# Kernel optimization log

Measured on AMD Instinct MI355X. Metric: run time of the kernel, lower is better.

The kernel has to match this reference:

```python
import jax, jax.numpy as jnp
import numpy as np
import math

D_MODEL = 512
DIM_K = 512
DIM_V = 512
N_HEADS = 8
B, S = 2, 2048


def setup_inputs() -> dict:
    key = jax.random.key(0)
    ks = jax.random.split(key, 10)
    s = 1.0 / math.sqrt(D_MODEL)
    return {
        "x": jax.random.normal(ks[0], (B, S, D_MODEL), jnp.float32),
        "y": jax.random.normal(ks[1], (B, S, D_MODEL), jnp.float32),
        # torch nn.Linear weights: [out, in]
        "q_w": jax.random.normal(ks[2], (DIM_K, D_MODEL), jnp.float32) * s,
        "q_b": jax.random.normal(ks[3], (DIM_K,), jnp.float32) * s,
        "k_w": jax.random.normal(ks[4], (DIM_K, D_MODEL), jnp.float32) * s,
        "k_b": jax.random.normal(ks[5], (DIM_K,), jnp.float32) * s,
        "v_w": jax.random.normal(ks[6], (DIM_V, D_MODEL), jnp.float32) * s,
        "v_b": jax.random.normal(ks[7], (DIM_V,), jnp.float32) * s,
        "o_w": jax.random.normal(ks[8], (D_MODEL, DIM_V), jnp.float32) * s,
        "o_b": jax.random.normal(ks[9], (D_MODEL,), jnp.float32) * s,
    }


def reference(x, y, q_w, q_b, k_w, k_b, v_w, v_b, o_w, o_b):
    b, s, _ = x.shape
    hd_k = DIM_K // N_HEADS
    hd_v = DIM_V // N_HEADS
    norm_fact = 1.0 / math.sqrt(D_MODEL)  # note: original scales by 1/sqrt(d_model)
    # torch code reshapes the flat [B,S,dim] projection row-major into [H,B,S,hd]
    Q = (x @ q_w.T + q_b).reshape(N_HEADS, b, s, hd_k)
    K = (y @ k_w.T + k_b).reshape(N_HEADS, b, s, hd_k)
    V = (y @ v_w.T + v_b).reshape(N_HEADS, b, s, hd_v)
    # scores: [H, B, Sq, Sk]
    scores = jnp.einsum("hbqd,hbkd->hbqk", Q, K) * norm_fact
    # per-row mean threshold: mask (set -inf) where score <= row mean
    thre = jnp.mean(scores, axis=-1, keepdims=True)
    scores = jnp.where(scores <= thre, -jnp.inf, scores)
    attn = jax.nn.softmax(scores, axis=-1)
    out = jnp.einsum("hbqk,hbkd->hbqd", attn, V).reshape(b, s, DIM_V)
    return out @ o_w.T + o_b
```

## Files before the change

### kernel.cpp

```cpp
#include <hip/hip_runtime.h>


typedef unsigned short ushort;
typedef unsigned int uint;

typedef __bf16  bf16x8   __attribute__((ext_vector_type(8)));
typedef float   floatx4  __attribute__((ext_vector_type(4)));
typedef float   floatx16 __attribute__((ext_vector_type(16)));
typedef float   float4v  __attribute__((ext_vector_type(4)));
typedef uint    uint4v   __attribute__((ext_vector_type(4)));
typedef ushort  ushort4v __attribute__((ext_vector_type(4)));

#define MFMA16(a,b,c) __builtin_amdgcn_mfma_f32_16x16x32_bf16((a),(b),(c),0,0,0)
#define MFMA32(a,b,c) __builtin_amdgcn_mfma_f32_32x32x16_bf16((a),(b),(c),0,0,0)

__device__ __forceinline__ float b2f(ushort u){
  union { uint i; float f; } v; v.i = ((uint)u) << 16; return v.f;
}
__device__ __forceinline__ ushort f2b(float f){
  union { float f; uint i; } v; v.f = f;
  uint r = v.i + 0x7FFFu + ((v.i >> 16) & 1u);
  return (ushort)(r >> 16);
}
__device__ __forceinline__ void split2(float f, ushort& h, ushort& l){
  h = f2b(f);
  l = f2b(f - b2f(h));
}
__device__ __forceinline__ void gload16(const ushort* g, ushort* l){
  __builtin_amdgcn_global_load_lds(
      (const __attribute__((address_space(1))) unsigned int*)g,
      (__attribute__((address_space(3))) unsigned int*)l, 16, 0, 0);
}

__global__ __launch_bounds__(256) void split_all(
    const float* __restrict__ x, const float* __restrict__ y,
    const float* __restrict__ qw, const float* __restrict__ kw,
    const float* __restrict__ vw, const float* __restrict__ ow,
    ushort* __restrict__ xhi, ushort* __restrict__ xlo,
    ushort* __restrict__ yhi, ushort* __restrict__ ylo,
    ushort* __restrict__ qwh, ushort* __restrict__ qwl,
    ushort* __restrict__ kwh, ushort* __restrict__ kwl,
    ushort* __restrict__ vwh, ushort* __restrict__ owh)
{
  int idx = blockIdx.x * 256 + threadIdx.x;
  if (idx < 1048576){
    const float* sp; ushort *hp, *lp; int i;
    if (idx < 524288){ sp = x; hp = xhi; lp = xlo; i = idx; }
    else             { sp = y; hp = yhi; lp = ylo; i = idx - 524288; }
    float4v d = ((const float4v*)sp)[i];
    ushort4v h, l;
    #pragma unroll
    for (int j=0;j<4;j++){ ushort hh,ll; split2(d[j],hh,ll); h[j]=hh; l[j]=ll; }
    ((ushort4v*)hp)[i] = h;
    ((ushort4v*)lp)[i] = l;
  } else {
    int k = idx - 1048576;
    int a = k >> 16, i = k & 65535;
    if (a < 2){
      const float* sp = a ? kw : qw;
      ushort *hp = a ? kwh : qwh, *lp = a ? kwl : qwl;
      float4v d = ((const float4v*)sp)[i];
      ushort4v h, l;
      #pragma unroll
      for (int j=0;j<4;j++){ ushort hh,ll; split2(d[j],hh,ll); h[j]=hh; l[j]=ll; }
      ((ushort4v*)hp)[i] = h;
      ((ushort4v*)lp)[i] = l;
    } else {
      const float* sp = (a == 2) ? vw : ow;
      ushort *hp = (a == 2) ? vwh : owh;
      float4v d = ((const float4v*)sp)[i];
      ushort4v h;
      #pragma unroll
      for (int j=0;j<4;j++) h[j] = f2b(d[j]);
      ((ushort4v*)hp)[i] = h;
    }
  }
}

__global__ __launch_bounds__(256) void proj_qkv(
    const ushort* __restrict__ xhi, const ushort* __restrict__ xlo,
    const ushort* __restrict__ yhi, const ushort* __restrict__ ylo,
    const ushort* __restrict__ qwh, const ushort* __restrict__ qwl,
    const ushort* __restrict__ kwh, const ushort* __restrict__ kwl,
    const ushort* __restrict__ vwh,
    const float* __restrict__ q_b, const float* __restrict__ k_b,
    const float* __restrict__ v_b,
    ushort* __restrict__ pq_hi, ushort* __restrict__ pq_lo,
    ushort* __restrict__ pk_hi, ushort* __restrict__ pk_lo,
    ushort* __restrict__ pv, float* __restrict__ ksum_out)
{
  const int seg = blockIdx.x >> 9;
  const int id  = blockIdx.x & 511;
  const int m0 = ((id & 7) * 8 + ((id >> 3) & 7)) * 64;
  const int n0 = (id >> 6) * 64;
  const bool split = (seg < 2);

  const ushort* Ahi = (seg == 0) ? xhi : yhi;
  const ushort* Alo = (seg == 0) ? xlo : ylo;
  const ushort* Bhi = (seg == 0) ? qwh : ((seg == 1) ? kwh : vwh);
  const ushort* Blo = (seg == 0) ? qwl : kwl;
  const float*  bias = (seg == 0) ? q_b : ((seg == 1) ? k_b : v_b);
  ushort* outhi = (seg == 0) ? pq_hi : ((seg == 1) ? pk_hi : pv);
  ushort* outlo = (seg == 0) ? pq_lo : pk_lo;

  __shared__ __align__(16) ushort AH[2][4096];
  __shared__ __align__(16) ushort AL[2][4096];
  __shared__ __align__(16) ushort BH[2][4096];
  __shared__ __align__(16) ushort BL[2][4096];
  __shared__ float cs[64];

  const int t    = threadIdx.x;
  const int lane = t & 63;
  const int w    = t >> 6;
  const int wm   = w >> 1, wn = w & 1;
  const int lr   = lane & 15, lg = lane >> 4;

  const int rl  = lane >> 3;
  const int c8s = (lane & 7) ^ rl;

  auto stage = [&](int buf, int k0){
    if (split){
      #pragma unroll
      for (int j = 0; j < 8; j++){
        const int c = w * 8 + j;
        if (c < 8)
          gload16(Ahi + (size_t)(m0 + c*8 + rl)*512 + k0 + c8s*8, &AH[buf][c*512]);
        else if (c < 16)
          gload16(Alo + (size_t)(m0 + (c-8)*8 + rl)*512 + k0 + c8s*8, &AL[buf][(c-8)*512]);
        else if (c < 24)
          gload16(Bhi + (size_t)(n0 + (c-16)*8 + rl)*512 + k0 + c8s*8, &BH[buf][(c-16)*512]);
        else
          gload16(Blo + (size_t)(n0 + (c-24)*8 + rl)*512 + k0 + c8s*8, &BL[buf][(c-24)*512]);
      }
    } else {
      #pragma unroll
      for (int j = 0; j < 4; j++){
        const int c = w * 4 + j;
        if (c < 8)
          gload16(Ahi + (size_t)(m0 + c*8 + rl)*512 + k0 + c8s*8, &AH[buf][c*512]);
        else
          gload16(Bhi + (size_t)(n0 + (c-8)*8 + rl)*512 + k0 + c8s*8, &BH[buf][(c-8)*512]);
      }
    }
  };

  floatx4 zf; zf[0]=0.f; zf[1]=0.f; zf[2]=0.f; zf[3]=0.f;
  floatx4 acc[2][2];
  #pragma unroll
  for (int i=0;i<2;i++)
    #pragma unroll
    for (int j=0;j<2;j++) acc[i][j] = zf;

  stage(0, 0);
  __syncthreads();

  int cur = 0;
  for (int it = 0; it < 8; ++it){
    if (it < 7) stage(cur^1, (it+1)*64);

    #pragma unroll
    for (int ks=0; ks<2; ks++){
      const int xo = ((ks*4 + lg) ^ (lr & 7)) << 3;
      bf16x8 ah[2], al[2], bh[2], bl[2];
      #pragma unroll
      for (int mi=0;mi<2;mi++){
        const int off = (wm*32 + mi*16 + lr)*64 + xo;
        ah[mi] = *(const bf16x8*)&AH[cur][off];
        if (split) al[mi] = *(const bf16x8*)&AL[cur][off];
      }
      #pragma unroll
      for (int ni=0;ni<2;ni++){
        const int off = (wn*32 + ni*16 + lr)*64 + xo;
        bh[ni] = *(const bf16x8*)&BH[cur][off];
        if (split) bl[ni] = *(const bf16x8*)&BL[cur][off];
      }
      #pragma unroll
      for (int mi=0;mi<2;mi++)
        #pragma unroll
        for (int ni=0;ni<2;ni++){
          acc[mi][ni] = MFMA16(ah[mi], bh[ni], acc[mi][ni]);
          if (split){
            acc[mi][ni] = MFMA16(ah[mi], bl[ni], acc[mi][ni]);
            acc[mi][ni] = MFMA16(al[mi], bh[ni], acc[mi][ni]);
          }
        }
    }
    __syncthreads();
    cur ^= 1;
  }

  #pragma unroll
  for (int ni=0;ni<2;ni++){
    const int n = n0 + wn*32 + ni*16 + lr;
    const float bn = bias[n];
    #pragma unroll
    for (int mi=0;mi<2;mi++){
      #pragma unroll
      for (int r=0;r<4;r++){
        const int m = m0 + wm*32 + mi*16 + lg*4 + r;
        const float c = acc[mi][ni][r] + bn;
        const size_t off = (size_t)m*512 + n;
        if (split){ ushort h,l; split2(c,h,l); outhi[off]=h; outlo[off]=l; }
        else      { outhi[off] = f2b(c); }
      }
    }
  }

  if (seg == 1) {
    if (t < 64) cs[t] = 0.f;
    __syncthreads();
    #pragma unroll
    for (int ni=0;ni<2;ni++){
      float s = 0.f;
      #pragma unroll
      for (int mi=0;mi<2;mi++)
        #pragma unroll
        for (int r=0;r<4;r++) s += acc[mi][ni][r];
      atomicAdd(&cs[wn*32 + ni*16 + lr], s);
    }
    __syncthreads();
    if (t < 64){
      const int hb = m0 >> 8;
      atomicAdd(&ksum_out[hb*64 + t], cs[t] + 64.f * bias[n0 + t]);
    }
  }
}

__global__ __launch_bounds__(256) void vtrans(
    const ushort* __restrict__ pv, ushort* __restrict__ vt)
{
  const int hb = blockIdx.y;
  const int s0 = blockIdx.x * 64;
  const size_t cb = (size_t)hb * 131072;
  __shared__ __align__(16) ushort T[64][68];
  const int t = threadIdx.x;
  {
    int s = t >> 2, c = (t & 3) * 16;
    *(uint4v*)&T[s][c]     = *(const uint4v*)&pv[cb + (size_t)(s0+s)*64 + c];
    *(uint4v*)&T[s][c + 8] = *(const uint4v*)&pv[cb + (size_t)(s0+s)*64 + c + 8];
  }
  __syncthreads();
  const int d = t >> 2, sc = (t & 3) * 16;
  ushort buf[16];
  #pragma unroll
  for (int i=0;i<16;i++) buf[i] = T[sc + i][d];
  *(uint4v*)&vt[cb + (size_t)d*2048 + s0 + sc]     = *(const uint4v*)&buf[0];
  *(uint4v*)&vt[cb + (size_t)d*2048 + s0 + sc + 8] = *(const uint4v*)&buf[8];
}

__device__ __forceinline__ void stage_tile(
    ushort* khb, ushort* klb, ushort* vtb,
    const ushort* gkhi, const ushort* gklo, const ushort* gvt,
    size_t cb, int kvb, int w, int l)
{
  const int rsub = l >> 3;
  const int c8   = (l & 7) ^ rsub;
  #pragma unroll
  for (int j = 0; j < 6; j++){
    const int chunk = w*6 + j;
    const int a   = chunk >> 3;
    const int sub = chunk & 7;
    const int row = sub*8 + rsub;
    if (a == 0)
      gload16(gkhi + cb + (size_t)(kvb + row)*64 + c8*8, khb + sub*512);
    else if (a == 1)
      gload16(gklo + cb + (size_t)(kvb + row)*64 + c8*8, klb + sub*512);
    else
      gload16(gvt  + cb + (size_t)row*2048 + kvb + c8*8, vtb + sub*512);
  }
}

__global__ __launch_bounds__(256) void attn_kernel(
    const ushort* __restrict__ qhi, const ushort* __restrict__ qlo,
    const ushort* __restrict__ khi, const ushort* __restrict__ klo,
    const ushort* __restrict__ vt,  const float* __restrict__ ksum,
    ushort* __restrict__ Obase, float* __restrict__ zbase)
{
  const int id = blockIdx.x;
  const int hb = ((id & 7) << 1) | ((id >> 3) & 1);
  const int kv = (id >> 4) & 1;
  const int q0 = (id >> 5) * 128;
  const size_t cb = (size_t)hb * 131072;
  const float C1 = 0.04419417382415922f * 1.44269504088896f;

  __shared__ __align__(16) ushort SMEM[24576];

  const int t = threadIdx.x, l = t & 63, w = t >> 6;
  const int lq = l & 31, h = l >> 5;
  const int kbase = kv * 1024;

  ushort* op = Obase + (size_t)kv * 2097152;
  float*  zp = zbase + kv * 32768;

  stage_tile(SMEM, SMEM + 8192, SMEM + 16384, khi, klo, vt, cb, kbase, w, l);

  union U8 { bf16x8 v; ushort u[8]; };
  U8 qfh[4], qfl[4];
  float part = 0.f;
  #pragma unroll
  for (int st=0; st<4; st++){
    size_t g = cb + (size_t)(q0 + w*32 + lq)*64 + st*16 + h*8;
    qfh[st].v = *(const bf16x8*)&qhi[g];
    qfl[st].v = *(const bf16x8*)&qlo[g];
    float4v k0 = *(const float4v*)&ksum[hb*64 + st*16 + h*8];
    float4v k1 = *(const float4v*)&ksum[hb*64 + st*16 + h*8 + 4];
    #pragma unroll
    for (int j=0;j<4;j++) part += (b2f(qfh[st].u[j])   + b2f(qfl[st].u[j]))   * k0[j];
    #pragma unroll
    for (int j=0;j<4;j++) part += (b2f(qfh[st].u[4+j]) + b2f(qfl[st].u[4+j])) * k1[j];
  }
  part += __shfl_xor(part, 32);
  const float rm = part * (1.f/2048.f);
  const float nrmc = -rm * C1;

  floatx16 O0 = {0,0,0,0,0,0,0,0,0,0,0,0,0,0,0,0};
  floatx16 O1 = O0;
  float za_r = 0.f, zb_r = 0.f;

  __syncthreads();

  int cur = 0;
  for (int kt = 0; kt < 16; kt++){
    if (kt + 1 < 16)
      stage_tile(SMEM + (cur^1)*4096, SMEM + 8192 + (cur^1)*4096,
                 SMEM + 16384 + (cur^1)*4096,
                 khi, klo, vt, cb, kbase + (kt+1)*64, w, l);

    const ushort* KHc = SMEM + cur*4096;
    const ushort* KLc = SMEM + 8192 + cur*4096;
    const ushort* VTc = SMEM + 16384 + cur*4096;

    floatx16 s0 = {0,0,0,0,0,0,0,0,0,0,0,0,0,0,0,0};
    floatx16 s1 = s0;
    __builtin_amdgcn_s_setprio(1);
    #pragma unroll
    for (int st=0; st<4; st++){
      const int xo = (((st*2 + h) ^ (lq & 7)) << 3);
      bf16x8 kh0 = *(const bf16x8*)&KHc[(lq     )*64 + xo];
      bf16x8 kl0 = *(const bf16x8*)&KLc[(lq     )*64 + xo];
      bf16x8 kh1 = *(const bf16x8*)&KHc[(32 + lq)*64 + xo];
      bf16x8 kl1 = *(const bf16x8*)&KLc[(32 + lq)*64 + xo];
      s0 = MFMA32(kh0, qfh[st].v, s0);
      s1 = MFMA32(kh1, qfh[st].v, s1);
      s0 = MFMA32(kh0, qfl[st].v, s0);
      s1 = MFMA32(kh1, qfl[st].v, s1);
      s0 = MFMA32(kl0, qfh[st].v, s0);
      s1 = MFMA32(kl1, qfh[st].v, s1);
    }
    __builtin_amdgcn_s_setprio(0);

    #pragma unroll
    for (int r=0;r<16;r++){
      float t0 = __builtin_fmaf(s0[r], C1, nrmc);
      float t1 = __builtin_fmaf(s1[r], C1, nrmc);
      float e0 = __builtin_amdgcn_exp2f(t0);
      float e1 = __builtin_amdgcn_exp2f(t1);
      e0 = (t0 > 0.f) ? e0 : 0.f;
      e1 = (t1 > 0.f) ? e1 : 0.f;
      za_r += e0; zb_r += e1;
      s0[r] = e0; s1[r] = e1;
    }

    bf16x8 pa[4];
    #pragma unroll
    for (int g=0; g<2; g++){
      const floatx16& sp = g ? s1 : s0;
      #pragma unroll
      for (int sg=0; sg<2; sg++){
        uint X0,X1,X2,X3;
        asm("v_cvt_pk_bf16_f32 %0, %1, %2" : "=v"(X0) : "v"(sp[sg*8+0]), "v"(sp[sg*8+1]));
        asm("v_cvt_pk_bf16_f32 %0, %1, %2" : "=v"(X1) : "v"(sp[sg*8+2]), "v"(sp[sg*8+3]));
        asm("v_cvt_pk_bf16_f32 %0, %1, %2" : "=v"(X2) : "v"(sp[sg*8+4]), "v"(sp[sg*8+5]));
        asm("v_cvt_pk_bf16_f32 %0, %1, %2" : "=v"(X3) : "v"(sp[sg*8+6]), "v"(sp[sg*8+7]));
        asm("v_permlane32_swap_b32 %0, %1" : "+v"(X0), "+v"(X2));
        asm("v_permlane32_swap_b32 %0, %1" : "+v"(X1), "+v"(X3));
        union { uint u[4]; bf16x8 v; } pu;
        pu.u[0]=X0; pu.u[1]=X1; pu.u[2]=X2; pu.u[3]=X3;
        pa[g*2+sg] = pu.v;
      }
    }

    __builtin_amdgcn_s_setprio(1);
    #pragma unroll
    for (int s4=0; s4<4; s4++){
      const int xo = (((s4*2 + h) ^ (lq & 7)) << 3);
      bf16x8 vf0 = *(const bf16x8*)&VTc[(lq     )*64 + xo];
      bf16x8 vf1 = *(const bf16x8*)&VTc[(32 + lq)*64 + xo];
      O0 = MFMA32(pa[s4], vf0, O0);
      O1 = MFMA32(pa[s4], vf1, O1);
    }
    __builtin_amdgcn_s_setprio(0);

    __syncthreads();
    cur ^= 1;
  }

  float zacc = za_r + zb_r;
  zacc += __shfl_xor(zacc, 32);
  if (h == 0) zp[hb*2048 + q0 + w*32 + l] = zacc;
  #pragma unroll
  for (int r=0;r<16;r++){
    const int crow = (r&3) + ((r>>2)<<3) + (h<<2);
    const int q = q0 + w*32 + crow;
    const size_t base = cb + (size_t)q*64 + lq;
    op[base]      = f2b(O0[r]);
    op[base + 32] = f2b(O1[r]);
  }
}

__global__ __launch_bounds__(256) void proj_out(
    const ushort* __restrict__ Obase, const float* __restrict__ zbase,
    const ushort* __restrict__ owh, const float* __restrict__ o_b,
    float* __restrict__ outf)
{
  const int id = blockIdx.x;
  const int m0 = ((id & 7) * 8 + ((id >> 3) & 7)) * 64;
  const int n0 = (id >> 6) * 64;

  __shared__ __align__(16) ushort AH[2][4096];
  __shared__ __align__(16) ushort BH[2][4096];

  const int t    = threadIdx.x;
  const int lane = t & 63;
  const int w    = t >> 6;
  const int wm   = w >> 1, wn = w & 1;
  const int lr   = lane & 15, lg = lane >> 4;

  const int rl  = lane >> 3;
  const int c8s = (lane & 7) ^ rl;

  auto stageB = [&](int buf, int k0){
    #pragma unroll
    for (int j = 0; j < 2; j++){
      const int c = w*2 + j;
      gload16(owh + (size_t)(n0 + c*8 + rl)*512 + k0 + c8s*8, &BH[buf][c*512]);
    }
  };

  const int ar = t >> 2, ac = t & 3;
  uint4v la[2][2];
  auto issueA = [&](int k0){
    const size_t base = (size_t)(m0 + ar)*512 + k0 + ac*16;
    #pragma unroll
    for (int p2=0;p2<2;p2++){
      la[p2][0] = *(const uint4v*)&Obase[(size_t)p2*2097152 + base];
      la[p2][1] = *(const uint4v*)&Obase[(size_t)p2*2097152 + base + 8];
    }
  };
  auto writeA = [&](int buf, int k0){
    const int m = m0 + ar;
    const int zq = (m >> 8)*2048 + (m & 255)*8 + (k0 >> 6);
    const float zi = 1.f / (zbase[zq] + zbase[32768 + zq]);
    uint4v o0, o1;
    #pragma unroll
    for (int j=0;j<4;j++){
      float lo0=0.f, hi0=0.f, lo1=0.f, hi1=0.f;
      #pragma unroll
      for (int p2=0;p2<2;p2++){
        lo0 += b2f((ushort)(la[p2][0][j] & 0xffff));
        hi0 += b2f((ushort)(la[p2][0][j] >> 16));
        lo1 += b2f((ushort)(la[p2][1][j] & 0xffff));
        hi1 += b2f((ushort)(la[p2][1][j] >> 16));
      }
      o0[j] = (uint)f2b(lo0*zi) | ((uint)f2b(hi0*zi) << 16);
      o1[j] = (uint)f2b(lo1*zi) | ((uint)f2b(hi1*zi) << 16);
    }
    const int p0 = ar*64 + (((ac*2    ) ^ (ar & 7)) << 3);
    const int p1 = ar*64 + (((ac*2 + 1) ^ (ar & 7)) << 3);
    *(uint4v*)&AH[buf][p0] = o0;
    *(uint4v*)&AH[buf][p1] = o1;
  };

  floatx4 zf; zf[0]=0.f; zf[1]=0.f; zf[2]=0.f; zf[3]=0.f;
  floatx4 acc[2][2];
  #pragma unroll
  for (int i=0;i<2;i++)
    #pragma unroll
    for (int j=0;j<2;j++) acc[i][j] = zf;

  issueA(0);
  stageB(0, 0);
  writeA(0, 0);
  __syncthreads();

  int cur = 0;
  for (int it = 0; it < 8; ++it){
    if (it < 7){ issueA((it+1)*64); stageB(cur^1, (it+1)*64); }

    #pragma unroll
    for (int ks=0; ks<2; ks++){
      const int xo = ((ks*4 + lg) ^ (lr & 7)) << 3;
      bf16x8 ah[2], bh[2];
      #pragma unroll
      for (int mi=0;mi<2;mi++)
        ah[mi] = *(const bf16x8*)&AH[cur][(wm*32 + mi*16 + lr)*64 + xo];
      #pragma unroll
      for (int ni=0;ni<2;ni++)
        bh[ni] = *(const bf16x8*)&BH[cur][(wn*32 + ni*16 + lr)*64 + xo];
      #pragma unroll
      for (int mi=0;mi<2;mi++)
        #pragma unroll
        for (int ni=0;ni<2;ni++)
          acc[mi][ni] = MFMA16(ah[mi], bh[ni], acc[mi][ni]);
    }
    if (it < 7) writeA(cur^1, (it+1)*64);
    __syncthreads();
    cur ^= 1;
  }

  #pragma unroll
  for (int ni=0;ni<2;ni++){
    const int n = n0 + wn*32 + ni*16 + lr;
    const float bn = o_b[n];
    #pragma unroll
    for (int mi=0;mi<2;mi++){
      #pragma unroll
      for (int r=0;r<4;r++){
        const int m = m0 + wm*32 + mi*16 + lg*4 + r;
        outf[(size_t)m*512 + n] = acc[mi][ni][r] + bn;
      }
    }
  }
}

extern "C" void kernel_launch(void* const* d_in, const int* in_sizes, int n_in,
                              void* d_out, int out_size, void* d_ws, size_t ws_size,
                              hipStream_t stream)
{
  const float* x   = (const float*)d_in[0];
  const float* y   = (const float*)d_in[1];
  const float* q_w = (const float*)d_in[2];
  const float* q_b = (const float*)d_in[3];
  const float* k_w = (const float*)d_in[4];
  const float* k_b = (const float*)d_in[5];
  const float* v_w = (const float*)d_in[6];
  const float* v_b = (const float*)d_in[7];
  const float* o_w = (const float*)d_in[8];
  const float* o_b = (const float*)d_in[9];

  const size_t NE = 4096ull * 512;
  const size_t WN = 512ull * 512;
  ushort* p = (ushort*)d_ws;
  ushort* pq_hi = p;
  ushort* pq_lo = pq_hi + NE;
  ushort* pk_hi = pq_lo + NE;
  ushort* pk_lo = pk_hi + NE;
  ushort* pv    = pk_lo + NE;
  ushort* xhi   = pv + NE;
  ushort* xlo   = xhi + NE;
  ushort* yhi   = xlo + NE;
  ushort* ylo   = yhi + NE;
  ushort* Obase = xhi;
  ushort* qwh = ylo + NE;
  ushort* qwl = qwh + WN;
  ushort* kwh = qwl + WN;
  ushort* kwl = kwh + WN;
  ushort* vwh = kwl + WN;
  ushort* owh = vwh + WN;
  float*  ksumb = (float*)(owh + WN);
  float*  zbase = ksumb + 1024;
  ushort* vtg   = (ushort*)(zbase + 2*32768);

  hipMemsetAsync(ksumb, 0, 16 * 64 * sizeof(float), stream);

  split_all<<<5120, 256, 0, stream>>>(x, y, q_w, k_w, v_w, o_w,
                                      xhi, xlo, yhi, ylo,
                                      qwh, qwl, kwh, kwl, vwh, owh);
  proj_qkv<<<1536, 256, 0, stream>>>(xhi, xlo, yhi, ylo,
                                     qwh, qwl, kwh, kwl, vwh,
                                     q_b, k_b, v_b,
                                     pq_hi, pq_lo, pk_hi, pk_lo, pv, ksumb);
  vtrans<<<dim3(32,16), 256, 0, stream>>>(pv, vtg);
  attn_kernel<<<512, 256, 0, stream>>>(pq_hi, pq_lo, pk_hi, pk_lo, vtg, ksumb,
                                       Obase, zbase);
  proj_out<<<512, 256, 0, stream>>>(Obase, zbase, owh, o_b, (float*)d_out);
}
```

Measured before the change: 110.5 us.

## Split attention keys four ways and interleave score/PV per half-tile

The attention kernel now splits the key range into four partitions instead of two, doubling the grid to 1024 blocks with 8 key tiles each. The per-tile loop handles 32 keys at a time: scores, exp and the PV MFMAs run per half-tile, so fewer accumulators are live. The kernel also gets a launch-bounds occupancy hint of 3. The aim is more parallel blocks and waves per CU to hide latency. The cost is that the output projection must read and sum four partial O buffers and four partial normalizers, which adds global memory traffic.

```diff
diff --git a/kernel.cpp b/kernel.cpp
--- a/kernel.cpp
+++ b/kernel.cpp
@@ -270,7 +270,7 @@
   }
 }
 
-__global__ __launch_bounds__(256) void attn_kernel(
+__global__ __launch_bounds__(256, 3) void attn_kernel(
     const ushort* __restrict__ qhi, const ushort* __restrict__ qlo,
     const ushort* __restrict__ khi, const ushort* __restrict__ klo,
     const ushort* __restrict__ vt,  const float* __restrict__ ksum,
@@ -278,8 +278,8 @@
 {
   const int id = blockIdx.x;
   const int hb = ((id & 7) << 1) | ((id >> 3) & 1);
-  const int kv = (id >> 4) & 1;
-  const int q0 = (id >> 5) * 128;
+  const int kv = (id >> 4) & 3;
+  const int q0 = (id >> 6) * 128;
   const size_t cb = (size_t)hb * 131072;
   const float C1 = 0.04419417382415922f * 1.44269504088896f;
 
@@ -287,7 +287,7 @@
 
   const int t = threadIdx.x, l = t & 63, w = t >> 6;
   const int lq = l & 31, h = l >> 5;
-  const int kbase = kv * 1024;
+  const int kbase = kv * 512;
 
   ushort* op = Obase + (size_t)kv * 2097152;
   float*  zp = zbase + kv * 32768;
@@ -315,13 +315,13 @@
 
   floatx16 O0 = {0,0,0,0,0,0,0,0,0,0,0,0,0,0,0,0};
   floatx16 O1 = O0;
-  float za_r = 0.f, zb_r = 0.f;
+  float zr = 0.f;
 
   __syncthreads();
 
   int cur = 0;
-  for (int kt = 0; kt < 16; kt++){
-    if (kt + 1 < 16)
+  for (int kt = 0; kt < 8; kt++){
+    if (kt + 1 < 8)
       stage_tile(SMEM + (cur^1)*4096, SMEM + 8192 + (cur^1)*4096,
                  SMEM + 16384 + (cur^1)*4096,
                  khi, klo, vt, cb, kbase + (kt+1)*64, w, l);
@@ -330,74 +330,67 @@
     const ushort* KLc = SMEM + 8192 + cur*4096;
     const ushort* VTc = SMEM + 16384 + cur*4096;
 
-    floatx16 s0 = {0,0,0,0,0,0,0,0,0,0,0,0,0,0,0,0};
-    floatx16 s1 = s0;
-    __builtin_amdgcn_s_setprio(1);
-    #pragma unroll
-    for (int st=0; st<4; st++){
-      const int xo = (((st*2 + h) ^ (lq & 7)) << 3);
-      bf16x8 kh0 = *(const bf16x8*)&KHc[(lq     )*64 + xo];
-      bf16x8 kl0 = *(const bf16x8*)&KLc[(lq     )*64 + xo];
-      bf16x8 kh1 = *(const bf16x8*)&KHc[(32 + lq)*64 + xo];
-      bf16x8 kl1 = *(const bf16x8*)&KLc[(32 + lq)*64 + xo];
-      s0 = MFMA32(kh0, qfh[st].v, s0);
-      s1 = MFMA32(kh1, qfh[st].v, s1);
-      s0 = MFMA32(kh0, qfl[st].v, s0);
-      s1 = MFMA32(kh1, qfl[st].v, s1);
-      s0 = MFMA32(kl0, qfh[st].v, s0);
-      s1 = MFMA32(kl1, qfh[st].v, s1);
-    }
-    __builtin_amdgcn_s_setprio(0);
-
-    #pragma unroll
-    for (int r=0;r<16;r++){
-      float t0 = __builtin_fmaf(s0[r], C1, nrmc);
-      float t1 = __builtin_fmaf(s1[r], C1, nrmc);
-      float e0 = __builtin_amdgcn_exp2f(t0);
-      float e1 = __builtin_amdgcn_exp2f(t1);
-      e0 = (t0 > 0.f) ? e0 : 0.f;
-      e1 = (t1 > 0.f) ? e1 : 0.f;
-      za_r += e0; zb_r += e1;
-      s0[r] = e0; s1[r] = e1;
-    }
-
-    bf16x8 pa[4];
     #pragma unroll
     for (int g=0; g<2; g++){
-      const floatx16& sp = g ? s1 : s0;
+      const int krow = g*32 + lq;
+
+      floatx16 sA = {0,0,0,0,0,0,0,0,0,0,0,0,0,0,0,0};
+      floatx16 sB = sA;
+      __builtin_amdgcn_s_setprio(1);
+      #pragma unroll
+      for (int st=0; st<4; st++){
+        const int xo = (((st*2 + h) ^ (lq & 7)) << 3);
+        bf16x8 kh = *(const bf16x8*)&KHc[krow*64 + xo];
+        bf16x8 kl2 = *(const bf16x8*)&KLc[krow*64 + xo];
+        sA = MFMA32(kh,  qfh[st].v, sA);
+        sB = MFMA32(kl2, qfh[st].v, sB);
+        sA = MFMA32(kh,  qfl[st].v, sA);
+      }
+      __builtin_amdgcn_s_setprio(0);
+
+      #pragma unroll
+      for (int r=0;r<16;r++){
+        float t0 = __builtin_fmaf(sA[r] + sB[r], C1, nrmc);
+        float e0 = __builtin_amdgcn_exp2f(t0);
+        e0 = (t0 > 0.f) ? e0 : 0.f;
+        zr += e0;
+        sA[r] = e0;
+      }
+
+      bf16x8 pa[2];
       #pragma unroll
       for (int sg=0; sg<2; sg++){
         uint X0,X1,X2,X3;
-        asm("v_cvt_pk_bf16_f32 %0, %1, %2" : "=v"(X0) : "v"(sp[sg*8+0]), "v"(sp[sg*8+1]));
-        asm("v_cvt_pk_bf16_f32 %0, %1, %2" : "=v"(X1) : "v"(sp[sg*8+2]), "v"(sp[sg*8+3]));
-        asm("v_cvt_pk_bf16_f32 %0, %1, %2" : "=v"(X2) : "v"(sp[sg*8+4]), "v"(sp[sg*8+5]));
-        asm("v_cvt_pk_bf16_f32 %0, %1, %2" : "=v"(X3) : "v"(sp[sg*8+6]), "v"(sp[sg*8+7]));
+        asm("v_cvt_pk_bf16_f32 %0, %1, %2" : "=v"(X0) : "v"(sA[sg*8+0]), "v"(sA[sg*8+1]));
+        asm("v_cvt_pk_bf16_f32 %0, %1, %2" : "=v"(X1) : "v"(sA[sg*8+2]), "v"(sA[sg*8+3]));
+        asm("v_cvt_pk_bf16_f32 %0, %1, %2" : "=v"(X2) : "v"(sA[sg*8+4]), "v"(sA[sg*8+5]));
+        asm("v_cvt_pk_bf16_f32 %0, %1, %2" : "=v"(X3) : "v"(sA[sg*8+6]), "v"(sA[sg*8+7]));
         asm("v_permlane32_swap_b32 %0, %1" : "+v"(X0), "+v"(X2));
         asm("v_permlane32_swap_b32 %0, %1" : "+v"(X1), "+v"(X3));
         union { uint u[4]; bf16x8 v; } pu;
         pu.u[0]=X0; pu.u[1]=X1; pu.u[2]=X2; pu.u[3]=X3;
-        pa[g*2+sg] = pu.v;
-      }
-    }
-
-    __builtin_amdgcn_s_setprio(1);
-    #pragma unroll
-    for (int s4=0; s4<4; s4++){
-      const int xo = (((s4*2 + h) ^ (lq & 7)) << 3);
-      bf16x8 vf0 = *(const bf16x8*)&VTc[(lq     )*64 + xo];
-      bf16x8 vf1 = *(const bf16x8*)&VTc[(32 + lq)*64 + xo];
-      O0 = MFMA32(pa[s4], vf0, O0);
-      O1 = MFMA32(pa[s4], vf1, O1);
-    }
-    __builtin_amdgcn_s_setprio(0);
+        pa[sg] = pu.v;
+      }
+
+      __builtin_amdgcn_s_setprio(1);
+      #pragma unroll
+      for (int sg=0; sg<2; sg++){
+        const int s4 = g*2 + sg;
+        const int xo = (((s4*2 + h) ^ (lq & 7)) << 3);
+        bf16x8 vf0 = *(const bf16x8*)&VTc[(lq     )*64 + xo];
+        bf16x8 vf1 = *(const bf16x8*)&VTc[(32 + lq)*64 + xo];
+        O0 = MFMA32(pa[sg], vf0, O0);
+        O1 = MFMA32(pa[sg], vf1, O1);
+      }
+      __builtin_amdgcn_s_setprio(0);
+    }
 
     __syncthreads();
     cur ^= 1;
   }
 
-  float zacc = za_r + zb_r;
-  zacc += __shfl_xor(zacc, 32);
-  if (h == 0) zp[hb*2048 + q0 + w*32 + l] = zacc;
+  zr += __shfl_xor(zr, 32);
+  if (h == 0) zp[hb*2048 + q0 + w*32 + l] = zr;
   #pragma unroll
   for (int r=0;r<16;r++){
     const int crow = (r&3) + ((r>>2)<<3) + (h<<2);
@@ -438,11 +431,11 @@
   };
 
   const int ar = t >> 2, ac = t & 3;
-  uint4v la[2][2];
+  uint4v la[4][2];
   auto issueA = [&](int k0){
     const size_t base = (size_t)(m0 + ar)*512 + k0 + ac*16;
     #pragma unroll
-    for (int p2=0;p2<2;p2++){
+    for (int p2=0;p2<4;p2++){
       la[p2][0] = *(const uint4v*)&Obase[(size_t)p2*2097152 + base];
       la[p2][1] = *(const uint4v*)&Obase[(size_t)p2*2097152 + base + 8];
     }
@@ -450,13 +443,16 @@
   auto writeA = [&](int buf, int k0){
     const int m = m0 + ar;
     const int zq = (m >> 8)*2048 + (m & 255)*8 + (k0 >> 6);
-    const float zi = 1.f / (zbase[zq] + zbase[32768 + zq]);
+    float zs = 0.f;
+    #pragma unroll
+    for (int p2=0;p2<4;p2++) zs += zbase[p2*32768 + zq];
+    const float zi = 1.f / zs;
     uint4v o0, o1;
     #pragma unroll
     for (int j=0;j<4;j++){
       float lo0=0.f, hi0=0.f, lo1=0.f, hi1=0.f;
       #pragma unroll
-      for (int p2=0;p2<2;p2++){
+      for (int p2=0;p2<4;p2++){
         lo0 += b2f((ushort)(la[p2][0][j] & 0xffff));
         hi0 += b2f((ushort)(la[p2][0][j] >> 16));
         lo1 += b2f((ushort)(la[p2][1][j] & 0xffff));
@@ -559,7 +555,7 @@
   ushort* owh = vwh + WN;
   float*  ksumb = (float*)(owh + WN);
   float*  zbase = ksumb + 1024;
-  ushort* vtg   = (ushort*)(zbase + 2*32768);
+  ushort* vtg   = (ushort*)(zbase + 4*32768);
 
   hipMemsetAsync(ksumb, 0, 16 * 64 * sizeof(float), stream);
 
@@ -571,7 +567,7 @@
                                      q_b, k_b, v_b,
                                      pq_hi, pq_lo, pk_hi, pk_lo, pv, ksumb);
   vtrans<<<dim3(32,16), 256, 0, stream>>>(pv, vtg);
-  attn_kernel<<<512, 256, 0, stream>>>(pq_hi, pq_lo, pk_hi, pk_lo, vtg, ksumb,
-                                       Obase, zbase);
+  attn_kernel<<<1024, 256, 0, stream>>>(pq_hi, pq_lo, pk_hi, pk_lo, vtg, ksumb,
+                                        Obase, zbase);
   proj_out<<<512, 256, 0, stream>>>(Obase, zbase, owh, o_b, (float*)d_out);
 }
```

After: 117.5 us. 1.06x slower.

## Merge split-K attention halves in-block via LDS and simplify output projection staging

Applied to the files above, without the earlier changes.

The attention kernel now runs both key halves inside one 512-thread block, with each group of four waves handling one half. The two partial outputs and row sums are combined through shared memory, and the kernel writes normalized bf16 output directly. This removes the separate partial-output and z buffers and the combine-plus-normalize work in proj_out, which now stages A straight from global memory with async loads. The trade-off is half as many blocks (256 on a large GPU), a larger LDS footprint, an extra barrier-based reduction, and removal of the s_setprio hints.

```diff
diff --git a/kernel.cpp b/kernel.cpp
--- a/kernel.cpp
+++ b/kernel.cpp
@@ -251,13 +251,13 @@
 __device__ __forceinline__ void stage_tile(
     ushort* khb, ushort* klb, ushort* vtb,
     const ushort* gkhi, const ushort* gklo, const ushort* gvt,
-    size_t cb, int kvb, int w, int l)
+    size_t cb, int kvb, int ws, int l)
 {
   const int rsub = l >> 3;
   const int c8   = (l & 7) ^ rsub;
   #pragma unroll
   for (int j = 0; j < 6; j++){
-    const int chunk = w*6 + j;
+    const int chunk = ws*6 + j;
     const int a   = chunk >> 3;
     const int sub = chunk & 7;
     const int row = sub*8 + rsub;
@@ -270,36 +270,34 @@
   }
 }
 
-__global__ __launch_bounds__(256) void attn_kernel(
+__global__ __launch_bounds__(512) void attn_kernel(
     const ushort* __restrict__ qhi, const ushort* __restrict__ qlo,
     const ushort* __restrict__ khi, const ushort* __restrict__ klo,
     const ushort* __restrict__ vt,  const float* __restrict__ ksum,
-    ushort* __restrict__ Obase, float* __restrict__ zbase)
+    ushort* __restrict__ attno)
 {
   const int id = blockIdx.x;
   const int hb = ((id & 7) << 1) | ((id >> 3) & 1);
-  const int kv = (id >> 4) & 1;
-  const int q0 = (id >> 5) * 128;
+  const int q0 = (id >> 4) * 128;
   const size_t cb = (size_t)hb * 131072;
   const float C1 = 0.04419417382415922f * 1.44269504088896f;
 
-  __shared__ __align__(16) ushort SMEM[24576];
+  __shared__ __align__(16) ushort TILES[2][2][3][4096];
 
   const int t = threadIdx.x, l = t & 63, w = t >> 6;
+  const int half = w >> 2, ws = w & 3;
   const int lq = l & 31, h = l >> 5;
-  const int kbase = kv * 1024;
-
-  ushort* op = Obase + (size_t)kv * 2097152;
-  float*  zp = zbase + kv * 32768;
-
-  stage_tile(SMEM, SMEM + 8192, SMEM + 16384, khi, klo, vt, cb, kbase, w, l);
+  const int kbase = half * 1024;
+
+  stage_tile(TILES[half][0][0], TILES[half][0][1], TILES[half][0][2],
+             khi, klo, vt, cb, kbase, ws, l);
 
   union U8 { bf16x8 v; ushort u[8]; };
   U8 qfh[4], qfl[4];
   float part = 0.f;
   #pragma unroll
   for (int st=0; st<4; st++){
-    size_t g = cb + (size_t)(q0 + w*32 + lq)*64 + st*16 + h*8;
+    size_t g = cb + (size_t)(q0 + ws*32 + lq)*64 + st*16 + h*8;
     qfh[st].v = *(const bf16x8*)&qhi[g];
     qfl[st].v = *(const bf16x8*)&qlo[g];
     float4v k0 = *(const float4v*)&ksum[hb*64 + st*16 + h*8];
@@ -315,24 +313,22 @@
 
   floatx16 O0 = {0,0,0,0,0,0,0,0,0,0,0,0,0,0,0,0};
   floatx16 O1 = O0;
-  float za_r = 0.f, zb_r = 0.f;
+  float za = 0.f, zb = 0.f;
 
   __syncthreads();
 
   int cur = 0;
   for (int kt = 0; kt < 16; kt++){
     if (kt + 1 < 16)
-      stage_tile(SMEM + (cur^1)*4096, SMEM + 8192 + (cur^1)*4096,
-                 SMEM + 16384 + (cur^1)*4096,
-                 khi, klo, vt, cb, kbase + (kt+1)*64, w, l);
-
-    const ushort* KHc = SMEM + cur*4096;
-    const ushort* KLc = SMEM + 8192 + cur*4096;
-    const ushort* VTc = SMEM + 16384 + cur*4096;
+      stage_tile(TILES[half][cur^1][0], TILES[half][cur^1][1], TILES[half][cur^1][2],
+                 khi, klo, vt, cb, kbase + (kt+1)*64, ws, l);
+
+    const ushort* KHc = TILES[half][cur][0];
+    const ushort* KLc = TILES[half][cur][1];
+    const ushort* VTc = TILES[half][cur][2];
 
     floatx16 s0 = {0,0,0,0,0,0,0,0,0,0,0,0,0,0,0,0};
     floatx16 s1 = s0;
-    __builtin_amdgcn_s_setprio(1);
     #pragma unroll
     for (int st=0; st<4; st++){
       const int xo = (((st*2 + h) ^ (lq & 7)) << 3);
@@ -347,7 +343,6 @@
       s0 = MFMA32(kl0, qfh[st].v, s0);
       s1 = MFMA32(kl1, qfh[st].v, s1);
     }
-    __builtin_amdgcn_s_setprio(0);
 
     #pragma unroll
     for (int r=0;r<16;r++){
@@ -357,7 +352,7 @@
       float e1 = __builtin_amdgcn_exp2f(t1);
       e0 = (t0 > 0.f) ? e0 : 0.f;
       e1 = (t1 > 0.f) ? e1 : 0.f;
-      za_r += e0; zb_r += e1;
+      za += e0; zb += e1;
       s0[r] = e0; s1[r] = e1;
     }
 
@@ -380,7 +375,6 @@
       }
     }
 
-    __builtin_amdgcn_s_setprio(1);
     #pragma unroll
     for (int s4=0; s4<4; s4++){
       const int xo = (((s4*2 + h) ^ (lq & 7)) << 3);
@@ -389,29 +383,40 @@
       O0 = MFMA32(pa[s4], vf0, O0);
       O1 = MFMA32(pa[s4], vf1, O1);
     }
-    __builtin_amdgcn_s_setprio(0);
 
     __syncthreads();
     cur ^= 1;
   }
 
-  float zacc = za_r + zb_r;
+  float zacc = za + zb;
   zacc += __shfl_xor(zacc, 32);
-  if (h == 0) zp[hb*2048 + q0 + w*32 + l] = zacc;
-  #pragma unroll
-  for (int r=0;r<16;r++){
-    const int crow = (r&3) + ((r>>2)<<3) + (h<<2);
-    const int q = q0 + w*32 + crow;
-    const size_t base = cb + (size_t)q*64 + lq;
-    op[base]      = f2b(O0[r]);
-    op[base + 32] = f2b(O1[r]);
+  float* CB = (float*)&TILES[0][0][0][0];
+  const int ci = (ws*64 + l)*34;
+  if (half == 1){
+    #pragma unroll
+    for (int i=0;i<16;i++){ CB[ci+i] = O0[i]; CB[ci+16+i] = O1[i]; }
+    CB[ci+32] = zacc;
+  }
+  __syncthreads();
+  if (half == 0){
+    const float zinv = 1.f / (zacc + CB[ci+32]);
+    #pragma unroll
+    for (int r=0;r<16;r++){ O0[r] += CB[ci+r]; O1[r] += CB[ci+16+r]; }
+    #pragma unroll
+    for (int r=0;r<16;r++){
+      const int crow = (r&3) + ((r>>2)<<3) + (h<<2);
+      const float zi = __shfl(zinv, crow);
+      const int q = q0 + ws*32 + crow;
+      const size_t base = cb + (size_t)q*64 + lq;
+      attno[base]      = f2b(O0[r] * zi);
+      attno[base + 32] = f2b(O1[r] * zi);
+    }
   }
 }
 
 __global__ __launch_bounds__(256) void proj_out(
-    const ushort* __restrict__ Obase, const float* __restrict__ zbase,
-    const ushort* __restrict__ owh, const float* __restrict__ o_b,
-    float* __restrict__ outf)
+    const ushort* __restrict__ attno, const ushort* __restrict__ owh,
+    const float* __restrict__ o_b, float* __restrict__ outf)
 {
   const int id = blockIdx.x;
   const int m0 = ((id & 7) * 8 + ((id >> 3) & 7)) * 64;
@@ -429,46 +434,15 @@
   const int rl  = lane >> 3;
   const int c8s = (lane & 7) ^ rl;
 
-  auto stageB = [&](int buf, int k0){
-    #pragma unroll
-    for (int j = 0; j < 2; j++){
-      const int c = w*2 + j;
-      gload16(owh + (size_t)(n0 + c*8 + rl)*512 + k0 + c8s*8, &BH[buf][c*512]);
-    }
-  };
-
-  const int ar = t >> 2, ac = t & 3;
-  uint4v la[2][2];
-  auto issueA = [&](int k0){
-    const size_t base = (size_t)(m0 + ar)*512 + k0 + ac*16;
-    #pragma unroll
-    for (int p2=0;p2<2;p2++){
-      la[p2][0] = *(const uint4v*)&Obase[(size_t)p2*2097152 + base];
-      la[p2][1] = *(const uint4v*)&Obase[(size_t)p2*2097152 + base + 8];
-    }
-  };
-  auto writeA = [&](int buf, int k0){
-    const int m = m0 + ar;
-    const int zq = (m >> 8)*2048 + (m & 255)*8 + (k0 >> 6);
-    const float zi = 1.f / (zbase[zq] + zbase[32768 + zq]);
-    uint4v o0, o1;
-    #pragma unroll
-    for (int j=0;j<4;j++){
-      float lo0=0.f, hi0=0.f, lo1=0.f, hi1=0.f;
-      #pragma unroll
-      for (int p2=0;p2<2;p2++){
-        lo0 += b2f((ushort)(la[p2][0][j] & 0xffff));
-        hi0 += b2f((ushort)(la[p2][0][j] >> 16));
-        lo1 += b2f((ushort)(la[p2][1][j] & 0xffff));
-        hi1 += b2f((ushort)(la[p2][1][j] >> 16));
-      }
-      o0[j] = (uint)f2b(lo0*zi) | ((uint)f2b(hi0*zi) << 16);
-      o1[j] = (uint)f2b(lo1*zi) | ((uint)f2b(hi1*zi) << 16);
-    }
-    const int p0 = ar*64 + (((ac*2    ) ^ (ar & 7)) << 3);
-    const int p1 = ar*64 + (((ac*2 + 1) ^ (ar & 7)) << 3);
-    *(uint4v*)&AH[buf][p0] = o0;
-    *(uint4v*)&AH[buf][p1] = o1;
+  auto stage = [&](int buf, int k0){
+    #pragma unroll
+    for (int j = 0; j < 4; j++){
+      const int c = w * 4 + j;
+      if (c < 8)
+        gload16(attno + (size_t)(m0 + c*8 + rl)*512 + k0 + c8s*8, &AH[buf][c*512]);
+      else
+        gload16(owh + (size_t)(n0 + (c-8)*8 + rl)*512 + k0 + c8s*8, &BH[buf][(c-8)*512]);
+    }
   };
 
   floatx4 zf; zf[0]=0.f; zf[1]=0.f; zf[2]=0.f; zf[3]=0.f;
@@ -478,14 +452,12 @@
     #pragma unroll
     for (int j=0;j<2;j++) acc[i][j] = zf;
 
-  issueA(0);
-  stageB(0, 0);
-  writeA(0, 0);
+  stage(0, 0);
   __syncthreads();
 
   int cur = 0;
   for (int it = 0; it < 8; ++it){
-    if (it < 7){ issueA((it+1)*64); stageB(cur^1, (it+1)*64); }
+    if (it < 7) stage(cur^1, (it+1)*64);
 
     #pragma unroll
     for (int ks=0; ks<2; ks++){
@@ -503,7 +475,6 @@
         for (int ni=0;ni<2;ni++)
           acc[mi][ni] = MFMA16(ah[mi], bh[ni], acc[mi][ni]);
     }
-    if (it < 7) writeA(cur^1, (it+1)*64);
     __syncthreads();
     cur ^= 1;
   }
@@ -550,7 +521,7 @@
   ushort* xlo   = xhi + NE;
   ushort* yhi   = xlo + NE;
   ushort* ylo   = yhi + NE;
-  ushort* Obase = xhi;
+  ushort* attno = xhi;
   ushort* qwh = ylo + NE;
   ushort* qwl = qwh + WN;
   ushort* kwh = qwl + WN;
@@ -558,8 +529,7 @@
   ushort* vwh = kwl + WN;
   ushort* owh = vwh + WN;
   float*  ksumb = (float*)(owh + WN);
-  float*  zbase = ksumb + 1024;
-  ushort* vtg   = (ushort*)(zbase + 2*32768);
+  ushort* vtg   = (ushort*)(ksumb + 1024);
 
   hipMemsetAsync(ksumb, 0, 16 * 64 * sizeof(float), stream);
 
@@ -571,7 +541,7 @@
                                      q_b, k_b, v_b,
                                      pq_hi, pq_lo, pk_hi, pk_lo, pv, ksumb);
   vtrans<<<dim3(32,16), 256, 0, stream>>>(pv, vtg);
-  attn_kernel<<<512, 256, 0, stream>>>(pq_hi, pq_lo, pk_hi, pk_lo, vtg, ksumb,
-                                       Obase, zbase);
-  proj_out<<<512, 256, 0, stream>>>(Obase, zbase, owh, o_b, (float*)d_out);
-}
+  attn_kernel<<<256, 512, 0, stream>>>(pq_hi, pq_lo, pk_hi, pk_lo, vtg, ksumb,
+                                       attno);
+  proj_out<<<512, 256, 0, stream>>>(attno, owh, o_b, (float*)d_out);
+}
```

After: 101.2 us. 8.3% less time.
